# Kernel tuning notes

Measured on AMD Instinct MI355X. Metric: run time of the kernel, lower is better.

The kernel has to match this reference:

```python
import jax, jax.numpy as jnp
import numpy as np

N = 50000
E = 500000
STRUCT = 128
SEM = 768
HID = 128
HEADS = 4


def setup_inputs() -> dict:
    key = jax.random.key(0)
    ks = jax.random.split(key, 16)
    rn = lambda k, s, sc=0.05: jax.random.normal(k, s, dtype=jnp.float32) * sc
    in_dim = STRUCT + SEM
    return {
        "x": rn(ks[0], (N, in_dim), 1.0),
        "edge_index": jax.random.randint(ks[1], (2, E), 0, N),
        "Wq": rn(ks[2], (STRUCT, HID)),
        "Wk": rn(ks[3], (SEM, HID)),
        "Wv": rn(ks[4], (SEM, HID)),
        "Wo": rn(ks[5], (STRUCT + HID, STRUCT)),
        "bo": jnp.zeros((STRUCT,), jnp.float32),
        "W1": rn(ks[6], (in_dim, HEADS * HID)),
        "att_src1": rn(ks[7], (HEADS, HID)),
        "att_dst1": rn(ks[8], (HEADS, HID)),
        "b1": jnp.zeros((HEADS * HID,), jnp.float32),
        "g1_w": jnp.ones((HEADS * HID,), jnp.float32),
        "g1_b": jnp.zeros((HEADS * HID,), jnp.float32),
        "g1_ms": jnp.ones((HEADS * HID,), jnp.float32),
        "W2": rn(ks[9], (HEADS * HID, HID)),
        "att_src2": rn(ks[10], (1, HID)),
        "att_dst2": rn(ks[11], (1, HID)),
        "b2": jnp.zeros((HID,), jnp.float32),
        "g2_w": jnp.ones((HID,), jnp.float32),
        "g2_b": jnp.zeros((HID,), jnp.float32),
        "g2_ms": jnp.ones((HID,), jnp.float32),
        "Wn": rn(ks[12], (HID, 2)),
        "bn": jnp.zeros((2,), jnp.float32),
    }


def gat_conv(x, src, dst, W, att_src, att_dst, bias, heads, out_c, concat):
    # PyG GATConv (self loops already appended to src/dst by caller)
    n = x.shape[0]
    h = (x @ W).reshape(n, heads, out_c)              # [N,H,C]
    a_src = (h * att_src).sum(-1)                      # [N,H]
    a_dst = (h * att_dst).sum(-1)                      # [N,H]
    alpha = jax.nn.leaky_relu(a_src[src] + a_dst[dst], 0.2)  # [Etot,H]
    amax = jax.ops.segment_max(alpha, dst, num_segments=n)
    amax = jnp.where(jnp.isfinite(amax), amax, 0.0)
    ex = jnp.exp(alpha - amax[dst])
    denom = jax.ops.segment_sum(ex, dst, num_segments=n)
    att = ex / (denom[dst] + 1e-16)                    # segment softmax over dst
    msg = h[src] * att[:, :, None]                     # [Etot,H,C]
    out = jax.ops.segment_sum(msg, dst, num_segments=n)
    out = out.reshape(n, heads * out_c) if concat else out.mean(1)
    return out + bias


def graph_norm(x, weight, bias, mean_scale, eps=1e-5):
    mean = x.mean(0, keepdims=True)
    out = x - mean * mean_scale
    var = (out * out).mean(0, keepdims=True)
    return out / jnp.sqrt(var + eps) * weight + bias


def reference(x, edge_index, Wq, Wk, Wv, Wo, bo, W1, att_src1, att_dst1, b1,
              g1_w, g1_b, g1_ms, W2, att_src2, att_dst2, b2, g2_w, g2_b, g2_ms,
              Wn, bn):
    x_struct = x[:, :STRUCT]
    x_sem = x[:, STRUCT:]
    # CrossModalFusion
    Q = x_struct @ Wq
    K = x_sem @ Wk
    V = x_sem @ Wv
    scores = (Q * K).sum(-1, keepdims=True)
    attn = jax.nn.sigmoid(scores) * V
    h0 = jnp.concatenate([x_struct, attn], axis=1) @ Wo + bo
    h = jnp.concatenate([h0, x_sem], axis=1)
    # add self loops once
    n = x.shape[0]
    loop = jnp.arange(n, dtype=edge_index.dtype)
    src = jnp.concatenate([edge_index[0], loop])
    dst = jnp.concatenate([edge_index[1], loop])
    h = gat_conv(h, src, dst, W1, att_src1, att_dst1, b1, HEADS, HID, True)
    h = jax.nn.elu(graph_norm(h, g1_w, g1_b, g1_ms))
    h = gat_conv(h, src, dst, W2, att_src2, att_dst2, b2, 1, HID, False)
    h = jax.nn.elu(graph_norm(h, g2_w, g2_b, g2_ms))
    return h @ Wn + bn
```

## Files before the change

kernel.cpp:

```cpp
#include <hip/hip_runtime.h>
#include <math.h>

#define NN 50000
#define NE 500000
#define EEDG 550000
#define SDIM 128
#define MDIM 768
#define HIDD 128
#define NHEADS 4
#define INDIM 896
#define H1D 512
#define SCAN_NB 196
#define MP 50048
#define MT 391

typedef unsigned short u16;
typedef unsigned int u32;
typedef __attribute__((ext_vector_type(8))) short short8;
typedef __attribute__((ext_vector_type(4))) float f32x4;

__device__ __forceinline__ u16 f2bf(float f) {
    union { float f; u32 u; } v; v.f = f;
    u32 r = v.u + 0x7FFFu + ((v.u >> 16) & 1u);
    return (u16)(r >> 16);
}
__device__ __forceinline__ float bf2f(u16 h) {
    union { u32 u; float f; } v; v.u = ((u32)h) << 16;
    return v.f;
}

__device__ __forceinline__ void gl_lds16(const u16* g, u16* l) {
    __builtin_amdgcn_global_load_lds(
        (const __attribute__((address_space(1))) void*)g,
        (__attribute__((address_space(3))) void*)l, 16, 0, 0);
}

__device__ __forceinline__ void edge_sd(const int* __restrict__ ei, int e, int& s, int& d) {
    if (e < NE) { s = ei[e]; d = ei[NE + e]; }
    else        { s = e - NE; d = e - NE; }
}

__global__ void fillk(float* __restrict__ p, float v, long count) {
    long i = (long)blockIdx.x * blockDim.x + threadIdx.x;
    long stride = (long)gridDim.x * blockDim.x;
    for (; i < count; i += stride) p[i] = v;
}

__global__ void fillk_i(int* __restrict__ p, int v, long count) {
    long i = (long)blockIdx.x * blockDim.x + threadIdx.x;
    long stride = (long)gridDim.x * blockDim.x;
    for (; i < count; i += stride) p[i] = v;
}

__global__ __launch_bounds__(256) void cast_pad_x(const float4* __restrict__ x4, u16* __restrict__ xb) {
    const long total = (long)MP * 224;
    long i = (long)blockIdx.x * blockDim.x + threadIdx.x;
    long stride = (long)gridDim.x * blockDim.x;
    for (; i < total; i += stride) {
        int row = (int)(i / 224);
        int c4 = (int)(i - (long)row * 224);
        float4 v = make_float4(0.f, 0.f, 0.f, 0.f);
        if (row < NN) v = x4[(size_t)row * 224 + c4];
        short4 o;
        o.x = (short)f2bf(v.x); o.y = (short)f2bf(v.y);
        o.z = (short)f2bf(v.z); o.w = (short)f2bf(v.w);
        *(short4*)(xb + (size_t)row * 896 + c4 * 4) = o;
    }
}

__global__ __launch_bounds__(256) void cast_wT(const float* __restrict__ W, u16* __restrict__ Wb, int K, int N) {
    int k = blockIdx.x * 4 + (threadIdx.x >> 6);
    int n = blockIdx.y * 64 + (threadIdx.x & 63);
    if (k < K && n < N) Wb[(size_t)n * K + k] = f2bf(W[(size_t)k * N + n]);
}

__global__ __launch_bounds__(256) void count_deg(const int* __restrict__ ei, int* __restrict__ deg) {
    int e = blockIdx.x * 256 + threadIdx.x;
    if (e >= EEDG) return;
    int d = e < NE ? ei[NE + e] : e - NE;
    atomicAdd(&deg[d], 1);
}

__global__ __launch_bounds__(256) void scan_bsum(const int* __restrict__ deg, int* __restrict__ part) {
    __shared__ int s[256];
    int t = threadIdx.x;
    int idx = blockIdx.x * 256 + t;
    s[t] = idx < NN ? deg[idx] : 0;
    __syncthreads();
    for (int off = 128; off; off >>= 1) {
        if (t < off) s[t] += s[t + off];
        __syncthreads();
    }
    if (t == 0) part[blockIdx.x] = s[0];
}

__global__ __launch_bounds__(256) void scan_part(int* __restrict__ part) {
    __shared__ int s[256];
    int t = threadIdx.x;
    int v = t < SCAN_NB ? part[t] : 0;
    s[t] = v;
    __syncthreads();
    for (int off = 1; off < 256; off <<= 1) {
        int x = t >= off ? s[t - off] : 0;
        __syncthreads();
        s[t] += x;
        __syncthreads();
    }
    if (t < SCAN_NB) part[t] = s[t] - v;
}

__global__ __launch_bounds__(256) void scan_write(const int* __restrict__ deg, const int* __restrict__ part,
                                                  int* __restrict__ rowptr) {
    __shared__ int s[256];
    int t = threadIdx.x;
    int idx = blockIdx.x * 256 + t;
    int v = idx < NN ? deg[idx] : 0;
    s[t] = v;
    __syncthreads();
    for (int off = 1; off < 256; off <<= 1) {
        int x = t >= off ? s[t - off] : 0;
        __syncthreads();
        s[t] += x;
        __syncthreads();
    }
    if (idx < NN) rowptr[idx] = part[blockIdx.x] + s[t] - v;
    if (idx == NN - 1) rowptr[NN] = EEDG;
}

__global__ __launch_bounds__(256) void fill_csr(const int* __restrict__ ei, const int* __restrict__ rowptr,
                                                int* __restrict__ cur, int* __restrict__ esrc,
                                                int* __restrict__ edst) {
    int e = blockIdx.x * 256 + threadIdx.x;
    if (e >= EEDG) return;
    int s, d;
    edge_sd(ei, e, s, d);
    int p = rowptr[d] + atomicAdd(&cur[d], 1);
    esrc[p] = s;
    edst[p] = d;
}

template<int H>
__global__ __launch_bounds__(256) void edge_exp(const int* __restrict__ esrc, const int* __restrict__ edst,
    const float* __restrict__ asrc, const float* __restrict__ adst, float* __restrict__ exf)
{
    int i = blockIdx.x * 256 + threadIdx.x;
    if (i >= EEDG) return;
    int s = esrc[i], d = edst[i];
    if (H == 4) {
        float4 as = *(const float4*)(asrc + s * 4);
        float4 ad = *(const float4*)(adst + d * 4);
        float4 o;
        float a;
        a = as.x + ad.x; a = a >= 0.f ? a : 0.2f * a; o.x = expf(a);
        a = as.y + ad.y; a = a >= 0.f ? a : 0.2f * a; o.y = expf(a);
        a = as.z + ad.z; a = a >= 0.f ? a : 0.2f * a; o.z = expf(a);
        a = as.w + ad.w; a = a >= 0.f ? a : 0.2f * a; o.w = expf(a);
        *(float4*)(exf + (size_t)i * 4) = o;
    } else {
        float a = asrc[s] + adst[d];
        a = a >= 0.f ? a : 0.2f * a;
        exf[i] = expf(a);
    }
}

template<int OUT_BF16>
__device__ __forceinline__ void gemm_body(
    u16* __restrict__ Asm, u16* __restrict__ Bsm,
    const u16* __restrict__ A1, int lda1, int K1,
    const u16* __restrict__ A2, int lda2, int K2,
    const u16* __restrict__ Bw,
    void* __restrict__ Cout, int ldc,
    const float* __restrict__ bias, int row0, int col0)
{
    const int tid = threadIdx.x;
    const int wave = tid >> 6, lane = tid & 63;
    const int wr = wave >> 1, wc = wave & 1;
    const int K = K1 + K2;
    const int srow = tid >> 2;
    const int skp = (tid & 3) * 8;
    const int l15 = lane & 15, l4 = lane >> 4;

    f32x4 acc[4][4];
    #pragma unroll
    for (int i = 0; i < 4; ++i)
        #pragma unroll
        for (int j = 0; j < 4; ++j)
            acc[i][j] = (f32x4){0.f, 0.f, 0.f, 0.f};

    for (int k0 = 0; k0 < K; k0 += 32) {
        const u16* Ab; int la; int kk;
        if (k0 < K1) { Ab = A1; la = lda1; kk = k0; }
        else         { Ab = A2; la = lda2; kk = k0 - K1; }
        gl_lds16(Ab + (size_t)(row0 + srow) * la + kk + skp,      Asm + srow * 32 + skp);
        gl_lds16(Ab + (size_t)(row0 + srow + 64) * la + kk + skp, Asm + (srow + 64) * 32 + skp);
        gl_lds16(Bw + (size_t)(col0 + srow) * K + k0 + skp,       Bsm + srow * 32 + skp);
        gl_lds16(Bw + (size_t)(col0 + srow + 64) * K + k0 + skp,  Bsm + (srow + 64) * 32 + skp);
        __syncthreads();
        short8 af[4], bfr[4];
        #pragma unroll
        for (int m = 0; m < 4; ++m)
            af[m] = *(const short8*)(Asm + (wr * 64 + m * 16 + l15) * 32 + l4 * 8);
        #pragma unroll
        for (int n = 0; n < 4; ++n)
            bfr[n] = *(const short8*)(Bsm + (wc * 64 + n * 16 + l15) * 32 + l4 * 8);
        #pragma unroll
        for (int m = 0; m < 4; ++m)
            #pragma unroll
            for (int n = 0; n < 4; ++n)
                acc[m][n] = __builtin_amdgcn_mfma_f32_16x16x32_bf16(af[m], bfr[n], acc[m][n], 0, 0, 0);
        __syncthreads();
    }
    #pragma unroll
    for (int m = 0; m < 4; ++m) {
        int r = row0 + wr * 64 + m * 16 + l4 * 4;
        #pragma unroll
        for (int n = 0; n < 4; ++n) {
            int c = col0 + wc * 64 + n * 16 + l15;
            float bv = bias ? bias[c] : 0.f;
            #pragma unroll
            for (int q = 0; q < 4; ++q) {
                float v = acc[m][n][q] + bv;
                if (OUT_BF16) ((u16*)Cout)[(size_t)(r + q) * ldc + c] = f2bf(v);
                else          ((float*)Cout)[(size_t)(r + q) * ldc + c] = v;
            }
        }
    }
}

template<int OUT_BF16>
__global__ __launch_bounds__(256) void gemm_mfma(
    const u16* __restrict__ A1, int lda1, int K1,
    const u16* __restrict__ A2, int lda2, int K2,
    const u16* __restrict__ Bw,
    void* __restrict__ Cout, int ldc,
    const float* __restrict__ bias)
{
    __shared__ u16 Asm[128 * 32];
    __shared__ u16 Bsm[128 * 32];
    gemm_body<OUT_BF16>(Asm, Bsm, A1, lda1, K1, A2, lda2, K2, Bw, Cout, ldc, bias,
                        blockIdx.y * 128, blockIdx.x * 128);
}

__global__ __launch_bounds__(256) void gemm_qkv(
    const u16* __restrict__ xb,
    const u16* __restrict__ wqT, const u16* __restrict__ wkT, const u16* __restrict__ wvT,
    u16* __restrict__ qb, u16* __restrict__ kb, u16* __restrict__ vb)
{
    __shared__ u16 Asm[128 * 32];
    __shared__ u16 Bsm[128 * 32];
    const u16* A; const u16* B; int K; u16* C;
    if (blockIdx.x == 0)      { A = xb;       B = wqT; K = 128; C = qb; }
    else if (blockIdx.x == 1) { A = xb + 128; B = wkT; K = 768; C = kb; }
    else                      { A = xb + 128; B = wvT; K = 768; C = vb; }
    gemm_body<1>(Asm, Bsm, A, 896, K, (const u16*)nullptr, 0, 0, B, C, 128, nullptr,
                 blockIdx.y * 128, 0);
}

__global__ __launch_bounds__(128) void node_attn_b(const u16* __restrict__ Q,
                                                   const u16* __restrict__ K,
                                                   u16* __restrict__ V)
{
    int nd = blockIdx.x;
    int t = threadIdx.x;
    size_t base = (size_t)nd * HIDD;
    float p = bf2f(Q[base + t]) * bf2f(K[base + t]);
    #pragma unroll
    for (int off = 32; off; off >>= 1) p += __shfl_down(p, off);
    __shared__ float sm[2];
    if ((t & 63) == 0) sm[t >> 6] = p;
    __syncthreads();
    float s = sm[0] + sm[1];
    float sig = 1.f / (1.f + expf(-s));
    V[base + t] = f2bf(bf2f(V[base + t]) * sig);
}

__global__ __launch_bounds__(256) void att_dots1_b(const u16* __restrict__ h1,
    const float* __restrict__ asv, const float* __restrict__ adv,
    float* __restrict__ a_src, float* __restrict__ a_dst)
{
    int nd = blockIdx.x;
    int t = threadIdx.x;
    int w = t >> 6, l = t & 63;
    const u16* hr = h1 + (size_t)nd * H1D + w * HIDD;
    const float* sv = asv + w * HIDD;
    const float* dv = adv + w * HIDD;
    float h0v = bf2f(hr[l]), h1v = bf2f(hr[l + 64]);
    float ps = h0v * sv[l] + h1v * sv[l + 64];
    float pd = h0v * dv[l] + h1v * dv[l + 64];
    #pragma unroll
    for (int off = 32; off; off >>= 1) {
        ps += __shfl_down(ps, off);
        pd += __shfl_down(pd, off);
    }
    if (l == 0) { a_src[nd * NHEADS + w] = ps; a_dst[nd * NHEADS + w] = pd; }
}

__global__ __launch_bounds__(128) void att_dots2_b(const u16* __restrict__ h2,
    const float* __restrict__ sv, const float* __restrict__ dv,
    float* __restrict__ a_src, float* __restrict__ a_dst)
{
    int nd = blockIdx.x;
    int t = threadIdx.x;
    float hv = bf2f(h2[(size_t)nd * HIDD + t]);
    float ps = hv * sv[t], pd = hv * dv[t];
    #pragma unroll
    for (int off = 32; off; off >>= 1) {
        ps += __shfl_down(ps, off);
        pd += __shfl_down(pd, off);
    }
    __shared__ float sm[4];
    if ((t & 63) == 0) { sm[t >> 6] = ps; sm[2 + (t >> 6)] = pd; }
    __syncthreads();
    if (t == 0) { a_src[nd] = sm[0] + sm[1]; a_dst[nd] = sm[2] + sm[3]; }
}

__global__ __launch_bounds__(256) void agg1_f(const int* __restrict__ rowptr, const int* __restrict__ esrc,
    const float* __restrict__ exf,
    const u16* __restrict__ h1b, const float* __restrict__ bias, u16* __restrict__ o1b)
{
    int d = blockIdx.x;
    int t = threadIdx.x;
    int c0 = t * 2;
    int h = t >> 6;
    int beg = rowptr[d], end = rowptr[d + 1];
    float n0 = 0.f, n1 = 0.f, den = 0.f;
    int i = beg;
    for (; i + 3 < end; i += 4) {
        int sA = esrc[i], sB = esrc[i + 1], sC = esrc[i + 2], sD = esrc[i + 3];
        float aA = exf[(size_t)i * 4 + h],       aB = exf[(size_t)(i + 1) * 4 + h];
        float aC = exf[(size_t)(i + 2) * 4 + h], aD = exf[(size_t)(i + 3) * 4 + h];
        u32 pA = *(const u32*)(h1b + (size_t)sA * H1D + c0);
        u32 pB = *(const u32*)(h1b + (size_t)sB * H1D + c0);
        u32 pC = *(const u32*)(h1b + (size_t)sC * H1D + c0);
        u32 pD = *(const u32*)(h1b + (size_t)sD * H1D + c0);
        den += (aA + aB) + (aC + aD);
        n0 = fmaf(bf2f((u16)pA), aA, n0);
        n1 = fmaf(bf2f((u16)(pA >> 16)), aA, n1);
        n0 = fmaf(bf2f((u16)pB), aB, n0);
        n1 = fmaf(bf2f((u16)(pB >> 16)), aB, n1);
        n0 = fmaf(bf2f((u16)pC), aC, n0);
        n1 = fmaf(bf2f((u16)(pC >> 16)), aC, n1);
        n0 = fmaf(bf2f((u16)pD), aD, n0);
        n1 = fmaf(bf2f((u16)(pD >> 16)), aD, n1);
    }
    for (; i < end; ++i) {
        int sA = esrc[i];
        float aA = exf[(size_t)i * 4 + h];
        u32 pA = *(const u32*)(h1b + (size_t)sA * H1D + c0);
        den += aA;
        n0 = fmaf(bf2f((u16)pA), aA, n0);
        n1 = fmaf(bf2f((u16)(pA >> 16)), aA, n1);
    }
    float invd = 1.f / (den + 1e-16f);
    float a0o = n0 * invd + bias[c0];
    float a1o = n1 * invd + bias[c0 + 1];
    u32 o = (u32)f2bf(a0o) | ((u32)f2bf(a1o) << 16);
    *(u32*)(o1b + (size_t)d * H1D + c0) = o;
}

__global__ __launch_bounds__(256) void agg2_f(const int* __restrict__ rowptr, const int* __restrict__ esrc,
    const float* __restrict__ exf,
    const u16* __restrict__ h2b, const float* __restrict__ bias, float* __restrict__ o2)
{
    int w = threadIdx.x >> 6, l = threadIdx.x & 63;
    int d = blockIdx.x * 4 + w;
    if (d >= NN) return;
    int c0 = l * 2;
    int beg = rowptr[d], end = rowptr[d + 1];
    float n0 = 0.f, n1 = 0.f, den = 0.f;
    int i = beg;
    for (; i + 3 < end; i += 4) {
        int sA = esrc[i], sB = esrc[i + 1], sC = esrc[i + 2], sD = esrc[i + 3];
        float aA = exf[i], aB = exf[i + 1], aC = exf[i + 2], aD = exf[i + 3];
        u32 pA = *(const u32*)(h2b + (size_t)sA * HIDD + c0);
        u32 pB = *(const u32*)(h2b + (size_t)sB * HIDD + c0);
        u32 pC = *(const u32*)(h2b + (size_t)sC * HIDD + c0);
        u32 pD = *(const u32*)(h2b + (size_t)sD * HIDD + c0);
        den += (aA + aB) + (aC + aD);
        n0 = fmaf(bf2f((u16)pA), aA, n0);
        n1 = fmaf(bf2f((u16)(pA >> 16)), aA, n1);
        n0 = fmaf(bf2f((u16)pB), aB, n0);
        n1 = fmaf(bf2f((u16)(pB >> 16)), aB, n1);
        n0 = fmaf(bf2f((u16)pC), aC, n0);
        n1 = fmaf(bf2f((u16)(pC >> 16)), aC, n1);
        n0 = fmaf(bf2f((u16)pD), aD, n0);
        n1 = fmaf(bf2f((u16)(pD >> 16)), aD, n1);
    }
    for (; i < end; ++i) {
        int sA = esrc[i];
        float aA = exf[i];
        u32 pA = *(const u32*)(h2b + (size_t)sA * HIDD + c0);
        den += aA;
        n0 = fmaf(bf2f((u16)pA), aA, n0);
        n1 = fmaf(bf2f((u16)(pA >> 16)), aA, n1);
    }
    float invd = 1.f / (den + 1e-16f);
    o2[(size_t)d * HIDD + c0]     = n0 * invd + bias[c0];
    o2[(size_t)d * HIDD + c0 + 1] = n1 * invd + bias[c0 + 1];
}

__global__ void colstat_b(const u16* __restrict__ x, float* __restrict__ msum,
                          float* __restrict__ vsum, int n, int rpb)
{
    int C = blockDim.x;
    int c = threadIdx.x;
    int r0 = blockIdx.x * rpb;
    int r1 = min(n, r0 + rpb);
    float s = 0.f, s2 = 0.f;
    for (int r = r0; r < r1; ++r) {
        float v = bf2f(x[(size_t)r * C + c]);
        s += v;
        s2 += v * v;
    }
    atomicAdd(&msum[c], s);
    atomicAdd(&vsum[c], s2);
}

__global__ void apply_norm_elu_b(u16* __restrict__ x, const float* __restrict__ msum,
                                 const float* __restrict__ vsum, const float* __restrict__ ms,
                                 const float* __restrict__ w, const float* __restrict__ b,
                                 int n, int rpb)
{
    int C = blockDim.x;
    int c = threadIdx.x;
    const float invn = 1.f / (float)NN;
    float mean = msum[c] * invn;
    float sub = mean * ms[c];
    float var = vsum[c] * invn - 2.f * sub * mean + sub * sub;
    float inv = rsqrtf(var + 1e-5f);
    float wc = w[c] * inv, bc = b[c];
    int r0 = blockIdx.x * rpb;
    int r1 = min(n, r0 + rpb);
    for (int r = r0; r < r1; ++r) {
        float v = (bf2f(x[(size_t)r * C + c]) - sub) * wc + bc;
        v = v > 0.f ? v : expm1f(v);
        x[(size_t)r * C + c] = f2bf(v);
    }
}

__global__ void colstat(const float* __restrict__ x, float* __restrict__ msum,
                        float* __restrict__ vsum, int n, int rpb)
{
    int C = blockDim.x;
    int c = threadIdx.x;
    int r0 = blockIdx.x * rpb;
    int r1 = min(n, r0 + rpb);
    float s = 0.f, s2 = 0.f;
    for (int r = r0; r < r1; ++r) {
        float v = x[(size_t)r * C + c];
        s += v;
        s2 += v * v;
    }
    atomicAdd(&msum[c], s);
    atomicAdd(&vsum[c], s2);
}

__global__ __launch_bounds__(128) void norm2_proj(const float* __restrict__ o2,
    const float* __restrict__ msum, const float* __restrict__ vsum,
    const float* __restrict__ ms, const float* __restrict__ w, const float* __restrict__ b,
    const float* __restrict__ Wn, const float* __restrict__ bn, float* __restrict__ out)
{
    int nd = blockIdx.x;
    int t = threadIdx.x;
    const float invn = 1.f / (float)NN;
    float mean = msum[t] * invn;
    float sub = mean * ms[t];
    float var = vsum[t] * invn - 2.f * sub * mean + sub * sub;
    float inv = rsqrtf(var + 1e-5f);
    float v = (o2[(size_t)nd * HIDD + t] - sub) * w[t] * inv + b[t];
    v = v > 0.f ? v : expm1f(v);
    float p0 = v * Wn[t * 2], p1 = v * Wn[t * 2 + 1];
    #pragma unroll
    for (int off = 32; off; off >>= 1) {
        p0 += __shfl_down(p0, off);
        p1 += __shfl_down(p1, off);
    }
    __shared__ float sm[4];
    if ((t & 63) == 0) { sm[t >> 6] = p0; sm[2 + (t >> 6)] = p1; }
    __syncthreads();
    if (t == 0) {
        out[nd * 2 + 0] = sm[0] + sm[1] + bn[0];
        out[nd * 2 + 1] = sm[2] + sm[3] + bn[1];
    }
}

extern "C" void kernel_launch(void* const* d_in, const int* in_sizes, int n_in,
                              void* d_out, int out_size, void* d_ws, size_t ws_size,
                              hipStream_t stream)
{
    const float* x   = (const float*)d_in[0];
    const int*   ei  = (const int*)d_in[1];
    const float* Wq  = (const float*)d_in[2];
    const float* Wk  = (const float*)d_in[3];
    const float* Wv  = (const float*)d_in[4];
    const float* Wo  = (const float*)d_in[5];
    const float* bo  = (const float*)d_in[6];
    const float* W1  = (const float*)d_in[7];
    const float* as1 = (const float*)d_in[8];
    const float* ad1 = (const float*)d_in[9];
    const float* b1  = (const float*)d_in[10];
    const float* g1w = (const float*)d_in[11];
    const float* g1b = (const float*)d_in[12];
    const float* g1m = (const float*)d_in[13];
    const float* W2  = (const float*)d_in[14];
    const float* as2 = (const float*)d_in[15];
    const float* ad2 = (const float*)d_in[16];
    const float* b2  = (const float*)d_in[17];
    const float* g2w = (const float*)d_in[18];
    const float* g2b = (const float*)d_in[19];
    const float* g2m = (const float*)d_in[20];
    const float* Wn  = (const float*)d_in[21];
    const float* bn  = (const float*)d_in[22];
    float* out = (float*)d_out;

    u16* usw = (u16*)d_ws;
    size_t uo = 0;
    u16* xb  = usw + uo; uo += (size_t)MP * 896;
    u16* h1b = usw + uo; uo += (size_t)MP * 512;
    u16* qb  = usw + uo; uo += (size_t)MP * 128;
    u16* kb  = usw + uo; uo += (size_t)MP * 128;
    u16* vb  = usw + uo; uo += (size_t)MP * 128;
    u16* o1b = usw + uo; uo += (size_t)MP * 512;
    u16* wqT = usw + uo; uo += 128 * 128;
    u16* wkT = usw + uo; uo += 128 * 768;
    u16* wvT = usw + uo; uo += 128 * 768;
    u16* woT = usw + uo; uo += 128 * 256;
    u16* w1T = usw + uo; uo += 512 * 896;
    u16* w2T = usw + uo; uo += 128 * 512;
    float* fws = (float*)(usw + uo);
    size_t fo = 0;
    float* asrc = fws + fo; fo += NN * NHEADS;
    float* adst = fws + fo; fo += NN * NHEADS;
    float* exf  = fws + fo; fo += (size_t)EEDG * NHEADS;
    float* msum = fws + fo; fo += 512;
    float* vsum = fws + fo; fo += 512;
    int* iws = (int*)(fws + fo);
    size_t io = 0;
    int* rowptr = iws + io; io += NN + 1;
    int* degcur = iws + io; io += 2 * NN;
    int* esrc   = iws + io; io += EEDG;
    int* edst   = iws + io; io += EEDG;
    int* spart  = iws + io; io += 256;
    int* cur    = degcur + NN;
    float* o2  = (float*)xb;
    u16* h0b = qb;
    u16* h2b = kb;

    const int EB = (EEDG + 255) / 256;

    cast_wT<<<dim3(32, 2),   256, 0, stream>>>(Wq, wqT, 128, 128);
    cast_wT<<<dim3(192, 2),  256, 0, stream>>>(Wk, wkT, 768, 128);
    cast_wT<<<dim3(192, 2),  256, 0, stream>>>(Wv, wvT, 768, 128);
    cast_wT<<<dim3(64, 2),   256, 0, stream>>>(Wo, woT, 256, 128);
    cast_wT<<<dim3(224, 8),  256, 0, stream>>>(W1, w1T, 896, 512);
    cast_wT<<<dim3(128, 2),  256, 0, stream>>>(W2, w2T, 512, 128);
    cast_pad_x<<<8192, 256, 0, stream>>>((const float4*)x, xb);

    fillk_i<<<392, 256, 0, stream>>>(degcur, 0, 2 * NN);
    count_deg<<<EB, 256, 0, stream>>>(ei, degcur);
    scan_bsum<<<SCAN_NB, 256, 0, stream>>>(degcur, spart);
    scan_part<<<1, 256, 0, stream>>>(spart);
    scan_write<<<SCAN_NB, 256, 0, stream>>>(degcur, spart, rowptr);
    fill_csr<<<EB, 256, 0, stream>>>(ei, rowptr, cur, esrc, edst);

    gemm_qkv<<<dim3(3, MT), 256, 0, stream>>>(xb, wqT, wkT, wvT, qb, kb, vb);
    node_attn_b<<<NN, 128, 0, stream>>>(qb, kb, vb);

    gemm_mfma<1><<<dim3(1, MT), 256, 0, stream>>>(xb, 896, 128, vb, 128, 128, woT, h0b, 128, bo);

    gemm_mfma<1><<<dim3(4, MT), 256, 0, stream>>>(h0b, 128, 128, xb + 128, 896, 768, w1T, h1b, 512, nullptr);

    att_dots1_b<<<NN, 256, 0, stream>>>(h1b, as1, ad1, asrc, adst);
    edge_exp<NHEADS><<<EB, 256, 0, stream>>>(esrc, edst, asrc, adst, exf);
    agg1_f<<<NN, 256, 0, stream>>>(rowptr, esrc, exf, h1b, b1, o1b);

    fillk<<<4, 256, 0, stream>>>(msum, 0.f, 1024);
    colstat_b<<<(NN + 127) / 128, H1D, 0, stream>>>(o1b, msum, vsum, NN, 128);
    apply_norm_elu_b<<<(NN + 127) / 128, H1D, 0, stream>>>(o1b, msum, vsum, g1m, g1w, g1b, NN, 128);

    gemm_mfma<1><<<dim3(1, MT), 256, 0, stream>>>(o1b, 512, 512, (const u16*)nullptr, 0, 0, w2T, h2b, 128, nullptr);
    att_dots2_b<<<NN, 128, 0, stream>>>(h2b, as2, ad2, asrc, adst);
    edge_exp<1><<<EB, 256, 0, stream>>>(esrc, edst, asrc, adst, exf);
    agg2_f<<<(NN + 3) / 4, 256, 0, stream>>>(rowptr, esrc, exf, h2b, b2, o2);

    fillk<<<4, 256, 0, stream>>>(msum, 0.f, 1024);
    colstat<<<(NN + 127) / 128, HIDD, 0, stream>>>(o2, msum, vsum, NN, 128);
    norm2_proj<<<NN, 128, 0, stream>>>(o2, msum, vsum, g2m, g2w, g2b, Wn, bn, out);
}
```

Before: 652.8 us.

## Fuse GAT attention dots into GEMM epilogues and merge setup kernels

Computes per-node attention source/destination dot products inside the MFMA GEMM epilogue via shuffle and shared-memory reduction, removing the separate att_dots kernels and the re-read of h1/h2. Merges the six weight transpose-cast kernels and the zero-fill kernels into one launch, and folds the msum reset into agg2. Widens the aggregation gather unroll from 4 to 8 edges for more memory-level parallelism. Adds epilogue work and register pressure to the GEMM, and pads the asrc/adst buffers to MP rows.

```diff
diff --git a/kernel.cpp b/kernel.cpp
--- a/kernel.cpp
+++ b/kernel.cpp
@@ -40,16 +40,32 @@
     else        { s = e - NE; d = e - NE; }
 }
 
-__global__ void fillk(float* __restrict__ p, float v, long count) {
-    long i = (long)blockIdx.x * blockDim.x + threadIdx.x;
-    long stride = (long)gridDim.x * blockDim.x;
-    for (; i < count; i += stride) p[i] = v;
-}
-
-__global__ void fillk_i(int* __restrict__ p, int v, long count) {
-    long i = (long)blockIdx.x * blockDim.x + threadIdx.x;
-    long stride = (long)gridDim.x * blockDim.x;
-    for (; i < count; i += stride) p[i] = v;
+__global__ __launch_bounds__(256) void cast_weights(
+    const float* __restrict__ Wq, const float* __restrict__ Wk, const float* __restrict__ Wv,
+    const float* __restrict__ Wo, const float* __restrict__ W1, const float* __restrict__ W2,
+    u16* __restrict__ wqT, u16* __restrict__ wkT, u16* __restrict__ wvT,
+    u16* __restrict__ woT, u16* __restrict__ w1T, u16* __restrict__ w2T,
+    int* __restrict__ degcur, float* __restrict__ msum)
+{
+    const int SQ = 128 * 128, SK = 128 * 768, SV = 128 * 768,
+              SO = 256 * 128, S1 = 896 * 512, S2 = 512 * 128;
+    long i = (long)blockIdx.x * 256 + threadIdx.x;
+    long w = i;
+    if (w < SQ) { int n = (int)(w / 128), k = (int)(w % 128); wqT[w] = f2bf(Wq[(size_t)k * 128 + n]); return; }
+    w -= SQ;
+    if (w < SK) { int n = (int)(w / 768), k = (int)(w % 768); wkT[w] = f2bf(Wk[(size_t)k * 128 + n]); return; }
+    w -= SK;
+    if (w < SV) { int n = (int)(w / 768), k = (int)(w % 768); wvT[w] = f2bf(Wv[(size_t)k * 128 + n]); return; }
+    w -= SV;
+    if (w < SO) { int n = (int)(w / 256), k = (int)(w % 256); woT[w] = f2bf(Wo[(size_t)k * 128 + n]); return; }
+    w -= SO;
+    if (w < S1) { int n = (int)(w / 896), k = (int)(w % 896); w1T[w] = f2bf(W1[(size_t)k * 512 + n]); return; }
+    w -= S1;
+    if (w < S2) { int n = (int)(w / 512), k = (int)(w % 512); w2T[w] = f2bf(W2[(size_t)k * 128 + n]); return; }
+    w -= S2;
+    if (w < 2 * NN) { degcur[w] = 0; return; }
+    w -= 2 * NN;
+    if (w < 1024) msum[w] = 0.f;
 }
 
 __global__ __launch_bounds__(256) void cast_pad_x(const float4* __restrict__ x4, u16* __restrict__ xb) {
@@ -66,12 +82,6 @@
         o.z = (short)f2bf(v.z); o.w = (short)f2bf(v.w);
         *(short4*)(xb + (size_t)row * 896 + c4 * 4) = o;
     }
-}
-
-__global__ __launch_bounds__(256) void cast_wT(const float* __restrict__ W, u16* __restrict__ Wb, int K, int N) {
-    int k = blockIdx.x * 4 + (threadIdx.x >> 6);
-    int n = blockIdx.y * 64 + (threadIdx.x & 63);
-    if (k < K && n < N) Wb[(size_t)n * K + k] = f2bf(W[(size_t)k * N + n]);
 }
 
 __global__ __launch_bounds__(256) void count_deg(const int* __restrict__ ei, int* __restrict__ deg) {
@@ -163,14 +173,16 @@
     }
 }
 
-template<int OUT_BF16>
+template<int OUT_BF16, int DOTS, int DH>
 __device__ __forceinline__ void gemm_body(
     u16* __restrict__ Asm, u16* __restrict__ Bsm,
     const u16* __restrict__ A1, int lda1, int K1,
     const u16* __restrict__ A2, int lda2, int K2,
     const u16* __restrict__ Bw,
     void* __restrict__ Cout, int ldc,
-    const float* __restrict__ bias, int row0, int col0)
+    const float* __restrict__ bias, int row0, int col0,
+    const float* __restrict__ dvs, const float* __restrict__ dvd,
+    float* __restrict__ aout_s, float* __restrict__ aout_d)
 {
     const int tid = threadIdx.x;
     const int wave = tid >> 6, lane = tid & 63;
@@ -225,20 +237,63 @@
             }
         }
     }
-}
-
-template<int OUT_BF16>
+    if (DOTS) {
+        const int head = (DH == 1) ? 0 : (col0 >> 7);
+        const float* svp = dvs + head * 128;
+        const float* dvp = dvd + head * 128;
+        float sv[4], dv[4];
+        #pragma unroll
+        for (int n = 0; n < 4; ++n) {
+            int cc = wc * 64 + n * 16 + l15;
+            sv[n] = svp[cc];
+            dv[n] = dvp[cc];
+        }
+        __shared__ float red[128][2][2];
+        #pragma unroll
+        for (int m = 0; m < 4; ++m) {
+            #pragma unroll
+            for (int q = 0; q < 4; ++q) {
+                float ps = 0.f, pd = 0.f;
+                #pragma unroll
+                for (int n = 0; n < 4; ++n) {
+                    ps = fmaf(acc[m][n][q], sv[n], ps);
+                    pd = fmaf(acc[m][n][q], dv[n], pd);
+                }
+                #pragma unroll
+                for (int off = 1; off < 16; off <<= 1) {
+                    ps += __shfl_xor(ps, off);
+                    pd += __shfl_xor(pd, off);
+                }
+                if (l15 == 0) {
+                    int lr = wr * 64 + m * 16 + l4 * 4 + q;
+                    red[lr][wc][0] = ps;
+                    red[lr][wc][1] = pd;
+                }
+            }
+        }
+        __syncthreads();
+        if (tid < 128) {
+            int r = row0 + tid;
+            aout_s[(size_t)r * DH + head] = red[tid][0][0] + red[tid][1][0];
+            aout_d[(size_t)r * DH + head] = red[tid][0][1] + red[tid][1][1];
+        }
+    }
+}
+
+template<int OUT_BF16, int DOTS, int DH>
 __global__ __launch_bounds__(256) void gemm_mfma(
     const u16* __restrict__ A1, int lda1, int K1,
     const u16* __restrict__ A2, int lda2, int K2,
     const u16* __restrict__ Bw,
     void* __restrict__ Cout, int ldc,
-    const float* __restrict__ bias)
+    const float* __restrict__ bias,
+    const float* __restrict__ dvs, const float* __restrict__ dvd,
+    float* __restrict__ aout_s, float* __restrict__ aout_d)
 {
     __shared__ u16 Asm[128 * 32];
     __shared__ u16 Bsm[128 * 32];
-    gemm_body<OUT_BF16>(Asm, Bsm, A1, lda1, K1, A2, lda2, K2, Bw, Cout, ldc, bias,
-                        blockIdx.y * 128, blockIdx.x * 128);
+    gemm_body<OUT_BF16, DOTS, DH>(Asm, Bsm, A1, lda1, K1, A2, lda2, K2, Bw, Cout, ldc, bias,
+                                  blockIdx.y * 128, blockIdx.x * 128, dvs, dvd, aout_s, aout_d);
 }
 
 __global__ __launch_bounds__(256) void gemm_qkv(
@@ -252,8 +307,8 @@
     if (blockIdx.x == 0)      { A = xb;       B = wqT; K = 128; C = qb; }
     else if (blockIdx.x == 1) { A = xb + 128; B = wkT; K = 768; C = kb; }
     else                      { A = xb + 128; B = wvT; K = 768; C = vb; }
-    gemm_body<1>(Asm, Bsm, A, 896, K, (const u16*)nullptr, 0, 0, B, C, 128, nullptr,
-                 blockIdx.y * 128, 0);
+    gemm_body<1, 0, 1>(Asm, Bsm, A, 896, K, (const u16*)nullptr, 0, 0, B, C, 128, nullptr,
+                       blockIdx.y * 128, 0, nullptr, nullptr, nullptr, nullptr);
 }
 
 __global__ __launch_bounds__(128) void node_attn_b(const u16* __restrict__ Q,
@@ -274,45 +329,13 @@
     V[base + t] = f2bf(bf2f(V[base + t]) * sig);
 }
 
-__global__ __launch_bounds__(256) void att_dots1_b(const u16* __restrict__ h1,
-    const float* __restrict__ asv, const float* __restrict__ adv,
-    float* __restrict__ a_src, float* __restrict__ a_dst)
-{
-    int nd = blockIdx.x;
-    int t = threadIdx.x;
-    int w = t >> 6, l = t & 63;
-    const u16* hr = h1 + (size_t)nd * H1D + w * HIDD;
-    const float* sv = asv + w * HIDD;
-    const float* dv = adv + w * HIDD;
-    float h0v = bf2f(hr[l]), h1v = bf2f(hr[l + 64]);
-    float ps = h0v * sv[l] + h1v * sv[l + 64];
-    float pd = h0v * dv[l] + h1v * dv[l + 64];
-    #pragma unroll
-    for (int off = 32; off; off >>= 1) {
-        ps += __shfl_down(ps, off);
-        pd += __shfl_down(pd, off);
-    }
-    if (l == 0) { a_src[nd * NHEADS + w] = ps; a_dst[nd * NHEADS + w] = pd; }
-}
-
-__global__ __launch_bounds__(128) void att_dots2_b(const u16* __restrict__ h2,
-    const float* __restrict__ sv, const float* __restrict__ dv,
-    float* __restrict__ a_src, float* __restrict__ a_dst)
-{
-    int nd = blockIdx.x;
-    int t = threadIdx.x;
-    float hv = bf2f(h2[(size_t)nd * HIDD + t]);
-    float ps = hv * sv[t], pd = hv * dv[t];
-    #pragma unroll
-    for (int off = 32; off; off >>= 1) {
-        ps += __shfl_down(ps, off);
-        pd += __shfl_down(pd, off);
-    }
-    __shared__ float sm[4];
-    if ((t & 63) == 0) { sm[t >> 6] = ps; sm[2 + (t >> 6)] = pd; }
-    __syncthreads();
-    if (t == 0) { a_src[nd] = sm[0] + sm[1]; a_dst[nd] = sm[2] + sm[3]; }
-}
+#define GATHER1(IDX, SS, AA) { \
+    int SS = esrc[IDX]; \
+    float AA = exf[(size_t)(IDX) * 4 + h]; \
+    u32 p_ = *(const u32*)(h1b + (size_t)SS * H1D + c0); \
+    den += AA; \
+    n0 = fmaf(bf2f((u16)p_), AA, n0); \
+    n1 = fmaf(bf2f((u16)(p_ >> 16)), AA, n1); }
 
 __global__ __launch_bounds__(256) void agg1_f(const int* __restrict__ rowptr, const int* __restrict__ esrc,
     const float* __restrict__ exf,
@@ -325,32 +348,32 @@
     int beg = rowptr[d], end = rowptr[d + 1];
     float n0 = 0.f, n1 = 0.f, den = 0.f;
     int i = beg;
-    for (; i + 3 < end; i += 4) {
-        int sA = esrc[i], sB = esrc[i + 1], sC = esrc[i + 2], sD = esrc[i + 3];
-        float aA = exf[(size_t)i * 4 + h],       aB = exf[(size_t)(i + 1) * 4 + h];
-        float aC = exf[(size_t)(i + 2) * 4 + h], aD = exf[(size_t)(i + 3) * 4 + h];
-        u32 pA = *(const u32*)(h1b + (size_t)sA * H1D + c0);
-        u32 pB = *(const u32*)(h1b + (size_t)sB * H1D + c0);
-        u32 pC = *(const u32*)(h1b + (size_t)sC * H1D + c0);
-        u32 pD = *(const u32*)(h1b + (size_t)sD * H1D + c0);
-        den += (aA + aB) + (aC + aD);
-        n0 = fmaf(bf2f((u16)pA), aA, n0);
-        n1 = fmaf(bf2f((u16)(pA >> 16)), aA, n1);
-        n0 = fmaf(bf2f((u16)pB), aB, n0);
-        n1 = fmaf(bf2f((u16)(pB >> 16)), aB, n1);
-        n0 = fmaf(bf2f((u16)pC), aC, n0);
-        n1 = fmaf(bf2f((u16)(pC >> 16)), aC, n1);
-        n0 = fmaf(bf2f((u16)pD), aD, n0);
-        n1 = fmaf(bf2f((u16)(pD >> 16)), aD, n1);
-    }
-    for (; i < end; ++i) {
-        int sA = esrc[i];
-        float aA = exf[(size_t)i * 4 + h];
-        u32 pA = *(const u32*)(h1b + (size_t)sA * H1D + c0);
-        den += aA;
-        n0 = fmaf(bf2f((u16)pA), aA, n0);
-        n1 = fmaf(bf2f((u16)(pA >> 16)), aA, n1);
-    }
+    for (; i + 7 < end; i += 8) {
+        int s0 = esrc[i], s1 = esrc[i+1], s2 = esrc[i+2], s3 = esrc[i+3];
+        int s4 = esrc[i+4], s5 = esrc[i+5], s6 = esrc[i+6], s7 = esrc[i+7];
+        float a0 = exf[(size_t)i*4+h],     a1 = exf[(size_t)(i+1)*4+h];
+        float a2 = exf[(size_t)(i+2)*4+h], a3 = exf[(size_t)(i+3)*4+h];
+        float a4 = exf[(size_t)(i+4)*4+h], a5 = exf[(size_t)(i+5)*4+h];
+        float a6 = exf[(size_t)(i+6)*4+h], a7 = exf[(size_t)(i+7)*4+h];
+        u32 p0 = *(const u32*)(h1b + (size_t)s0 * H1D + c0);
+        u32 p1 = *(const u32*)(h1b + (size_t)s1 * H1D + c0);
+        u32 p2 = *(const u32*)(h1b + (size_t)s2 * H1D + c0);
+        u32 p3 = *(const u32*)(h1b + (size_t)s3 * H1D + c0);
+        u32 p4 = *(const u32*)(h1b + (size_t)s4 * H1D + c0);
+        u32 p5 = *(const u32*)(h1b + (size_t)s5 * H1D + c0);
+        u32 p6 = *(const u32*)(h1b + (size_t)s6 * H1D + c0);
+        u32 p7 = *(const u32*)(h1b + (size_t)s7 * H1D + c0);
+        den += ((a0 + a1) + (a2 + a3)) + ((a4 + a5) + (a6 + a7));
+        n0 = fmaf(bf2f((u16)p0), a0, n0); n1 = fmaf(bf2f((u16)(p0 >> 16)), a0, n1);
+        n0 = fmaf(bf2f((u16)p1), a1, n0); n1 = fmaf(bf2f((u16)(p1 >> 16)), a1, n1);
+        n0 = fmaf(bf2f((u16)p2), a2, n0); n1 = fmaf(bf2f((u16)(p2 >> 16)), a2, n1);
+        n0 = fmaf(bf2f((u16)p3), a3, n0); n1 = fmaf(bf2f((u16)(p3 >> 16)), a3, n1);
+        n0 = fmaf(bf2f((u16)p4), a4, n0); n1 = fmaf(bf2f((u16)(p4 >> 16)), a4, n1);
+        n0 = fmaf(bf2f((u16)p5), a5, n0); n1 = fmaf(bf2f((u16)(p5 >> 16)), a5, n1);
+        n0 = fmaf(bf2f((u16)p6), a6, n0); n1 = fmaf(bf2f((u16)(p6 >> 16)), a6, n1);
+        n0 = fmaf(bf2f((u16)p7), a7, n0); n1 = fmaf(bf2f((u16)(p7 >> 16)), a7, n1);
+    }
+    for (; i < end; ++i) GATHER1(i, sA, aA)
     float invd = 1.f / (den + 1e-16f);
     float a0o = n0 * invd + bias[c0];
     float a1o = n1 * invd + bias[c0 + 1];
@@ -360,8 +383,15 @@
 
 __global__ __launch_bounds__(256) void agg2_f(const int* __restrict__ rowptr, const int* __restrict__ esrc,
     const float* __restrict__ exf,
-    const u16* __restrict__ h2b, const float* __restrict__ bias, float* __restrict__ o2)
-{
+    const u16* __restrict__ h2b, const float* __restrict__ bias, float* __restrict__ o2,
+    float* __restrict__ msum)
+{
+    if (blockIdx.x == 0) {
+        msum[threadIdx.x] = 0.f;
+        msum[threadIdx.x + 256] = 0.f;
+        msum[threadIdx.x + 512] = 0.f;
+        msum[threadIdx.x + 768] = 0.f;
+    }
     int w = threadIdx.x >> 6, l = threadIdx.x & 63;
     int d = blockIdx.x * 4 + w;
     if (d >= NN) return;
@@ -369,22 +399,28 @@
     int beg = rowptr[d], end = rowptr[d + 1];
     float n0 = 0.f, n1 = 0.f, den = 0.f;
     int i = beg;
-    for (; i + 3 < end; i += 4) {
-        int sA = esrc[i], sB = esrc[i + 1], sC = esrc[i + 2], sD = esrc[i + 3];
-        float aA = exf[i], aB = exf[i + 1], aC = exf[i + 2], aD = exf[i + 3];
-        u32 pA = *(const u32*)(h2b + (size_t)sA * HIDD + c0);
-        u32 pB = *(const u32*)(h2b + (size_t)sB * HIDD + c0);
-        u32 pC = *(const u32*)(h2b + (size_t)sC * HIDD + c0);
-        u32 pD = *(const u32*)(h2b + (size_t)sD * HIDD + c0);
-        den += (aA + aB) + (aC + aD);
-        n0 = fmaf(bf2f((u16)pA), aA, n0);
-        n1 = fmaf(bf2f((u16)(pA >> 16)), aA, n1);
-        n0 = fmaf(bf2f((u16)pB), aB, n0);
-        n1 = fmaf(bf2f((u16)(pB >> 16)), aB, n1);
-        n0 = fmaf(bf2f((u16)pC), aC, n0);
-        n1 = fmaf(bf2f((u16)(pC >> 16)), aC, n1);
-        n0 = fmaf(bf2f((u16)pD), aD, n0);
-        n1 = fmaf(bf2f((u16)(pD >> 16)), aD, n1);
+    for (; i + 7 < end; i += 8) {
+        int s0 = esrc[i], s1 = esrc[i+1], s2 = esrc[i+2], s3 = esrc[i+3];
+        int s4 = esrc[i+4], s5 = esrc[i+5], s6 = esrc[i+6], s7 = esrc[i+7];
+        float a0 = exf[i],   a1 = exf[i+1], a2 = exf[i+2], a3 = exf[i+3];
+        float a4 = exf[i+4], a5 = exf[i+5], a6 = exf[i+6], a7 = exf[i+7];
+        u32 p0 = *(const u32*)(h2b + (size_t)s0 * HIDD + c0);
+        u32 p1 = *(const u32*)(h2b + (size_t)s1 * HIDD + c0);
+        u32 p2 = *(const u32*)(h2b + (size_t)s2 * HIDD + c0);
+        u32 p3 = *(const u32*)(h2b + (size_t)s3 * HIDD + c0);
+        u32 p4 = *(const u32*)(h2b + (size_t)s4 * HIDD + c0);
+        u32 p5 = *(const u32*)(h2b + (size_t)s5 * HIDD + c0);
+        u32 p6 = *(const u32*)(h2b + (size_t)s6 * HIDD + c0);
+        u32 p7 = *(const u32*)(h2b + (size_t)s7 * HIDD + c0);
+        den += ((a0 + a1) + (a2 + a3)) + ((a4 + a5) + (a6 + a7));
+        n0 = fmaf(bf2f((u16)p0), a0, n0); n1 = fmaf(bf2f((u16)(p0 >> 16)), a0, n1);
+        n0 = fmaf(bf2f((u16)p1), a1, n0); n1 = fmaf(bf2f((u16)(p1 >> 16)), a1, n1);
+        n0 = fmaf(bf2f((u16)p2), a2, n0); n1 = fmaf(bf2f((u16)(p2 >> 16)), a2, n1);
+        n0 = fmaf(bf2f((u16)p3), a3, n0); n1 = fmaf(bf2f((u16)(p3 >> 16)), a3, n1);
+        n0 = fmaf(bf2f((u16)p4), a4, n0); n1 = fmaf(bf2f((u16)(p4 >> 16)), a4, n1);
+        n0 = fmaf(bf2f((u16)p5), a5, n0); n1 = fmaf(bf2f((u16)(p5 >> 16)), a5, n1);
+        n0 = fmaf(bf2f((u16)p6), a6, n0); n1 = fmaf(bf2f((u16)(p6 >> 16)), a6, n1);
+        n0 = fmaf(bf2f((u16)p7), a7, n0); n1 = fmaf(bf2f((u16)(p7 >> 16)), a7, n1);
     }
     for (; i < end; ++i) {
         int sA = esrc[i];
@@ -529,8 +565,8 @@
     u16* w2T = usw + uo; uo += 128 * 512;
     float* fws = (float*)(usw + uo);
     size_t fo = 0;
-    float* asrc = fws + fo; fo += NN * NHEADS;
-    float* adst = fws + fo; fo += NN * NHEADS;
+    float* asrc = fws + fo; fo += (size_t)MP * NHEADS;
+    float* adst = fws + fo; fo += (size_t)MP * NHEADS;
     float* exf  = fws + fo; fo += (size_t)EEDG * NHEADS;
     float* msum = fws + fo; fo += 512;
     float* vsum = fws + fo; fo += 512;
@@ -547,16 +583,13 @@
     u16* h2b = kb;
 
     const int EB = (EEDG + 255) / 256;
-
-    cast_wT<<<dim3(32, 2),   256, 0, stream>>>(Wq, wqT, 128, 128);
-    cast_wT<<<dim3(192, 2),  256, 0, stream>>>(Wk, wkT, 768, 128);
-    cast_wT<<<dim3(192, 2),  256, 0, stream>>>(Wv, wvT, 768, 128);
-    cast_wT<<<dim3(64, 2),   256, 0, stream>>>(Wo, woT, 256, 128);
-    cast_wT<<<dim3(224, 8),  256, 0, stream>>>(W1, w1T, 896, 512);
-    cast_wT<<<dim3(128, 2),  256, 0, stream>>>(W2, w2T, 512, 128);
+    const int CW_BLOCKS = (770048 + 2 * NN + 1024 + 255) / 256;
+
+    cast_weights<<<CW_BLOCKS, 256, 0, stream>>>(Wq, Wk, Wv, Wo, W1, W2,
+                                                wqT, wkT, wvT, woT, w1T, w2T,
+                                                degcur, msum);
     cast_pad_x<<<8192, 256, 0, stream>>>((const float4*)x, xb);
 
-    fillk_i<<<392, 256, 0, stream>>>(degcur, 0, 2 * NN);
     count_deg<<<EB, 256, 0, stream>>>(ei, degcur);
     scan_bsum<<<SCAN_NB, 256, 0, stream>>>(degcur, spart);
     scan_part<<<1, 256, 0, stream>>>(spart);
@@ -566,24 +599,23 @@
     gemm_qkv<<<dim3(3, MT), 256, 0, stream>>>(xb, wqT, wkT, wvT, qb, kb, vb);
     node_attn_b<<<NN, 128, 0, stream>>>(qb, kb, vb);
 
-    gemm_mfma<1><<<dim3(1, MT), 256, 0, stream>>>(xb, 896, 128, vb, 128, 128, woT, h0b, 128, bo);
-
-    gemm_mfma<1><<<dim3(4, MT), 256, 0, stream>>>(h0b, 128, 128, xb + 128, 896, 768, w1T, h1b, 512, nullptr);
-
-    att_dots1_b<<<NN, 256, 0, stream>>>(h1b, as1, ad1, asrc, adst);
+    gemm_mfma<1, 0, 1><<<dim3(1, MT), 256, 0, stream>>>(xb, 896, 128, vb, 128, 128, woT, h0b, 128, bo,
+                                                        nullptr, nullptr, nullptr, nullptr);
+
+    gemm_mfma<1, 1, 4><<<dim3(4, MT), 256, 0, stream>>>(h0b, 128, 128, xb + 128, 896, 768, w1T, h1b, 512,
+                                                        nullptr, as1, ad1, asrc, adst);
+
     edge_exp<NHEADS><<<EB, 256, 0, stream>>>(esrc, edst, asrc, adst, exf);
     agg1_f<<<NN, 256, 0, stream>>>(rowptr, esrc, exf, h1b, b1, o1b);
 
-    fillk<<<4, 256, 0, stream>>>(msum, 0.f, 1024);
     colstat_b<<<(NN + 127) / 128, H1D, 0, stream>>>(o1b, msum, vsum, NN, 128);
     apply_norm_elu_b<<<(NN + 127) / 128, H1D, 0, stream>>>(o1b, msum, vsum, g1m, g1w, g1b, NN, 128);
 
-    gemm_mfma<1><<<dim3(1, MT), 256, 0, stream>>>(o1b, 512, 512, (const u16*)nullptr, 0, 0, w2T, h2b, 128, nullptr);
-    att_dots2_b<<<NN, 128, 0, stream>>>(h2b, as2, ad2, asrc, adst);
+    gemm_mfma<1, 1, 1><<<dim3(1, MT), 256, 0, stream>>>(o1b, 512, 512, (const u16*)nullptr, 0, 0, w2T, h2b, 128,
+                                                        nullptr, as2, ad2, asrc, adst);
     edge_exp<1><<<EB, 256, 0, stream>>>(esrc, edst, asrc, adst, exf);
-    agg2_f<<<(NN + 3) / 4, 256, 0, stream>>>(rowptr, esrc, exf, h2b, b2, o2);
-
-    fillk<<<4, 256, 0, stream>>>(msum, 0.f, 1024);
+    agg2_f<<<(NN + 3) / 4, 256, 0, stream>>>(rowptr, esrc, exf, h2b, b2, o2, msum);
+
     colstat<<<(NN + 127) / 128, HIDD, 0, stream>>>(o2, msum, vsum, NN, 128);
     norm2_proj<<<NN, 128, 0, stream>>>(o2, msum, vsum, g2m, g2w, g2b, Wn, bn, out);
 }
```

Measured after the change: 635.3 us. 2.7% less time.
